# Kernel tuning notes

Hardware: AMD Instinct MI355X
Metric: run time of the kernel (lower is better)

The kernel has to match this reference:

```python
import jax, jax.numpy as jnp
import numpy as np

C = 256
CQK = C // 8  # query/key channels


def setup_inputs() -> dict:
    key = jax.random.key(0)
    ks = jax.random.split(key, 7)
    B, H, W = 4, 64, 64
    x = jax.random.normal(ks[0], (B, C, H, W), dtype=jnp.float32)
    # 1x1 conv weights stored as [out_ch, in_ch] (kernel spatial dims are 1)
    sc = 1.0 / np.sqrt(C)
    Wq = jax.random.uniform(ks[1], (CQK, C), jnp.float32, -sc, sc)
    bq = jax.random.uniform(ks[2], (CQK,), jnp.float32, -sc, sc)
    Wk = jax.random.uniform(ks[3], (CQK, C), jnp.float32, -sc, sc)
    bk = jax.random.uniform(ks[4], (CQK,), jnp.float32, -sc, sc)
    Wv = jax.random.uniform(ks[5], (C, C), jnp.float32, -sc, sc)
    bv = jax.random.uniform(ks[6], (C,), jnp.float32, -sc, sc)
    gamma = jnp.zeros((1,), dtype=jnp.float32)
    return {"x": x, "Wq": Wq, "bq": bq, "Wk": Wk, "bk": bk, "Wv": Wv, "bv": bv, "gamma": gamma}


def reference(x, Wq, bq, Wk, bk, Wv, bv, gamma):
    B, Ch, H, W = x.shape
    N = H * W
    xf = x.reshape(B, Ch, N)  # [B, C, N]
    # 1x1 convs == per-pixel linear projections
    q = jnp.einsum('oc,bcn->bno', Wq, xf) + bq  # [B, N, CQK]
    k = jnp.einsum('oc,bcn->bon', Wk, xf) + bk[None, :, None]  # [B, CQK, N]
    v = jnp.einsum('oc,bcn->bon', Wv, xf) + bv[None, :, None]  # [B, C, N]
    s = jnp.einsum('bnd,bdm->bnm', q, k)  # [B, N, N]
    attn = jax.nn.softmax(s, axis=-1)
    # out[b,c,i] = sum_j v[b,c,j] * attn[b,i,j]
    out = jnp.einsum('bcj,bij->bci', v, attn).reshape(B, Ch, H, W)
    return x + gamma[0] * out
```

## Files before the change

### kernel.cpp

```cpp
#include <hip/hip_runtime.h>
#include <math.h>

#define BATCH 4
#define CCH   256
#define DQK   32
#define NPIX  4096
#define LOG2E 1.44269504088896340736f

typedef __attribute__((ext_vector_type(8)))  short          short8_t;
typedef __attribute__((ext_vector_type(4)))  unsigned short ushort4_t;
typedef __attribute__((ext_vector_type(8)))  unsigned short ushort8_t;
typedef __attribute__((ext_vector_type(16))) float          f32x16;
typedef __attribute__((ext_vector_type(2)))  unsigned int   uint2_t;

#if __has_builtin(__builtin_amdgcn_exp2f)
#define EXP2F(x) __builtin_amdgcn_exp2f(x)
#else
#define EXP2F(x) exp2f(x)
#endif

#define MFMA32(a, b, c) __builtin_amdgcn_mfma_f32_32x32x16_bf16(a, b, c, 0, 0, 0)

static __device__ __forceinline__ unsigned short f2bf(float f) {
    union { float f; unsigned int u; } v; v.f = f;
    unsigned int r = v.u + 0x7FFFu + ((v.u >> 16) & 1u);
    return (unsigned short)(r >> 16);
}

static __device__ __forceinline__ short8_t cat8(ushort4_t a, ushort4_t b) {
    ushort8_t c = __builtin_shufflevector(a, b, 0, 1, 2, 3, 4, 5, 6, 7);
    short8_t r; __builtin_memcpy(&r, &c, 16); return r;
}

static __device__ __forceinline__ short8_t u4_to_s8(const unsigned int* u) {
    short8_t r; __builtin_memcpy(&r, u, 16); return r;
}

static __device__ __forceinline__ uint2_t plswap(unsigned int a, unsigned int b) {
#if __has_builtin(__builtin_amdgcn_permlane32_swap)
    return __builtin_amdgcn_permlane32_swap(a, b, false, false);
#else
    const unsigned int sa = (unsigned int)__shfl_xor((int)a, 32);
    const unsigned int sb = (unsigned int)__shfl_xor((int)b, 32);
    const int h = (threadIdx.x >> 5) & 1;
    uint2_t r;
    r.x = h ? sb : a;
    r.y = h ? b : sa;
    return r;
#endif
}

static __device__ __forceinline__ void make_bfrag(
    const f32x16& s, float& l0, float& l1, unsigned int bfr[2][4])
{
    float pv[16];
    #pragma unroll
    for (int r = 0; r < 16; ++r) pv[r] = EXP2F(s[r]);
    #pragma unroll
    for (int r = 0; r < 16; r += 2) { l0 += pv[r]; l1 += pv[r + 1]; }
    unsigned int P[8];
    #pragma unroll
    for (int v = 0; v < 8; ++v)
        P[v] = __builtin_amdgcn_perm(__float_as_uint(pv[2 * v + 1]),
                                     __float_as_uint(pv[2 * v]), 0x07060302u);
    #pragma unroll
    for (int kp = 0; kp < 2; ++kp) {
        const uint2_t r02 = plswap(P[4 * kp + 0], P[4 * kp + 2]);
        const uint2_t r13 = plswap(P[4 * kp + 1], P[4 * kp + 3]);
        bfr[kp][0] = r02.x; bfr[kp][1] = r13.x;
        bfr[kp][2] = r02.y; bfr[kp][3] = r13.y;
    }
}

__global__ __launch_bounds__(256) void wconv_kernel(
    const float* __restrict__ Wq, const float* __restrict__ Wk,
    const float* __restrict__ Wv, unsigned short* __restrict__ wbf)
{
    const int idx = blockIdx.x * 256 + threadIdx.x;
    const int o = idx >> 8, c = idx & 255;
    float v;
    if (o < 32)      v = Wq[o * 256 + c] * LOG2E;
    else if (o < 64) v = Wk[(o - 32) * 256 + c];
    else             v = Wv[(o - 64) * 256 + c];
    wbf[((c >> 3) * 320 + o) * 8 + (c & 7)] = f2bf(v);
}

__global__ __launch_bounds__(256) void xt_kernel(
    const float* __restrict__ x, unsigned short* __restrict__ xfrag)
{
    const int b  = blockIdx.x >> 6;
    const int cg = (blockIdx.x >> 4) & 3;
    const int ng = blockIdx.x & 15;
    const int t  = threadIdx.x;
    const int w = t >> 6, l = t & 63;

    #pragma unroll
    for (int sgl = 0; sgl < 2; ++sgl) {
        const int sg = w * 2 + sgl;
        float f[4][8];
        #pragma unroll
        for (int p = 0; p < 8; ++p) {
            const float* row = x + ((size_t)(b * CCH + cg * 64 + sg * 8 + p)) * NPIX
                                 + ng * 256;
            #pragma unroll
            for (int j = 0; j < 4; ++j)
                f[j][p] = row[j * 64 + l];
        }
        #pragma unroll
        for (int j = 0; j < 4; ++j) {
            unsigned int d[4];
            #pragma unroll
            for (int k = 0; k < 4; ++k)
                d[k] = __builtin_amdgcn_perm(__float_as_uint(f[j][2 * k + 1]),
                                             __float_as_uint(f[j][2 * k]), 0x07060302u);
            const int nt = ng * 8 + j * 2 + (l >> 5);
            unsigned short* dst = xfrag +
                ((((size_t)(b * 128 + nt) * 32) + cg * 8 + sg) * 32 + (l & 31)) * 8;
            *(short8_t*)dst = u4_to_s8(d);
        }
    }
}

__global__ __launch_bounds__(320) void proj_kernel(
    const unsigned short* __restrict__ xfrag, const unsigned short* __restrict__ wbf,
    const float* __restrict__ bq, const float* __restrict__ bk,
    const float* __restrict__ bv,
    unsigned short* __restrict__ qfrag, unsigned short* __restrict__ kfrag,
    unsigned short* __restrict__ vfrag)
{
    __shared__ unsigned short qkb[2 * 2 * 32 * 40];
    __shared__ unsigned short vbuf[4 * 64 * 72];

    const int b   = blockIdx.x >> 6;
    const int nt0 = (blockIdx.x & 63) << 1;
    const int t   = threadIdx.x;
    const int w = t >> 6, lane = t & 63, il = lane & 31, h = lane >> 5;

    float4 bA[4], bB[4];
    #pragma unroll
    for (int g = 0; g < 4; ++g) {
        if (w == 0) {
            bA[g] = *(const float4*)&bq[8 * g + 4 * h];
            bB[g] = *(const float4*)&bk[8 * g + 4 * h];
        } else {
            bA[g] = *(const float4*)&bv[(w - 1) * 64 + 8 * g + 4 * h];
            bB[g] = *(const float4*)&bv[(w - 1) * 64 + 32 + 8 * g + 4 * h];
        }
    }

    f32x16 acc[2][2];
    #pragma unroll
    for (int a = 0; a < 2; ++a)
        #pragma unroll
        for (int i = 0; i < 2; ++i)
            #pragma unroll
            for (int r = 0; r < 16; ++r) acc[a][i][r] = 0.f;

    const unsigned short* wp = wbf + ((size_t)(h * 320 + w * 64 + il)) * 8;
    const unsigned short* xp0 = xfrag + (((size_t)(b * 128 + nt0) * 32 + h) * 32 + il) * 8;
    const unsigned short* xp1 = xp0 + (size_t)32 * 32 * 8;

    #pragma unroll 4
    for (int ks = 0; ks < 16; ++ks) {
        const short8_t af0 = *(const short8_t*)(wp + ks * 5120);
        const short8_t af1 = *(const short8_t*)(wp + ks * 5120 + 256);
        const short8_t bf0 = *(const short8_t*)(xp0 + (size_t)ks * 2 * 256);
        const short8_t bf1 = *(const short8_t*)(xp1 + (size_t)ks * 2 * 256);
        acc[0][0] = MFMA32(af0, bf0, acc[0][0]);
        acc[0][1] = MFMA32(af0, bf1, acc[0][1]);
        acc[1][0] = MFMA32(af1, bf0, acc[1][0]);
        acc[1][1] = MFMA32(af1, bf1, acc[1][1]);
    }

    if (w == 0) {
        #pragma unroll
        for (int it = 0; it < 2; ++it)
            #pragma unroll
            for (int r = 0; r < 16; ++r) {
                const int d = (r & 3) + 8 * (r >> 2) + 4 * h;
                qkb[(it * 2 + 0) * 1280 + il * 40 + d] =
                    f2bf(acc[0][it][r] + bA[r >> 2][r & 3] * LOG2E);
                qkb[(it * 2 + 1) * 1280 + il * 40 + d] =
                    f2bf(acc[1][it][r] + bB[r >> 2][r & 3]);
            }
        #pragma unroll
        for (int it = 0; it < 2; ++it)
            #pragma unroll
            for (int rep = 0; rep < 2; ++rep) {
                const int u = rep * 64 + lane;
                const int slot = u >> 5, n = u & 31;
                ushort4_t qlo = *(const ushort4_t*)&qkb[(it * 2) * 1280 + n * 40 + slot * 8];
                ushort4_t qhi = *(const ushort4_t*)&qkb[(it * 2) * 1280 + n * 40 + slot * 8 + 4];
                ushort4_t klo = *(const ushort4_t*)&qkb[(it * 2 + 1) * 1280 + n * 40 + slot * 8];
                ushort4_t khi = *(const ushort4_t*)&qkb[(it * 2 + 1) * 1280 + n * 40 + slot * 8 + 4];
                const size_t o8 = (((size_t)(b * 128 + nt0 + it) * 4 + slot) * 32 + n) * 8;
                *(short8_t*)(qfrag + o8) = cat8(qlo, qhi);
                *(short8_t*)(kfrag + o8) = cat8(klo, khi);
            }
    } else {
        unsigned short* vb = vbuf + (w - 1) * 64 * 72;
        #pragma unroll
        for (int it = 0; it < 2; ++it)
            #pragma unroll
            for (int r = 0; r < 16; ++r) {
                const int orow = (r & 3) + 8 * (r >> 2) + 4 * h;
                vb[(orow)      * 72 + it * 32 + il] = f2bf(acc[0][it][r] + bA[r >> 2][r & 3]);
                vb[(orow + 32) * 72 + it * 32 + il] = f2bf(acc[1][it][r] + bB[r >> 2][r & 3]);
            }
        #pragma unroll
        for (int rep = 0; rep < 8; ++rep) {
            const int u = rep * 64 + lane;
            const int c = u & 63, m = u >> 6;
            const int it = m >> 2, slot = m & 3;
            ushort4_t lo = *(const ushort4_t*)&vb[c * 72 + it * 32 + slot * 8];
            ushort4_t hi = *(const ushort4_t*)&vb[c * 72 + it * 32 + slot * 8 + 4];
            const size_t o8 = (((size_t)(b * 128 + nt0 + it) * 4 + slot) * 256 +
                               (w - 1) * 64 + c) * 8;
            *(short8_t*)(vfrag + o8) = cat8(lo, hi);
        }
    }
}

struct KStage { short8_t k0, k1; };

__global__ __launch_bounds__(512, 2) void attn_kernel(
    const unsigned short* __restrict__ qfrag,
    const unsigned short* __restrict__ kfrag,
    const unsigned short* __restrict__ vfrag,
    const float* __restrict__ x,
    const float* __restrict__ gamma,
    float* __restrict__ out)
{
    __shared__ float comb[8][64][17];

    const int m8 = blockIdx.x & 7;
    const int b  = m8 >> 1;
    const int itile = ((blockIdx.x >> 3) << 1) | (m8 & 1);
    const int i0 = itile << 6;
    const int t  = threadIdx.x;
    const int w = t >> 6, lane = t & 63, il = lane & 31, h = lane >> 5;
    const int it = w & 1, ci = (w >> 1) & 1, jj = w >> 2;

    short8_t qf[2];
    #pragma unroll
    for (int ks = 0; ks < 2; ++ks)
        qf[ks] = *(const short8_t*)(qfrag +
            (((size_t)(b * 128 + itile * 2 + it) * 4 + ks * 2 + h) * 32 + il) * 8);

    const size_t kbase = (size_t)(b * 128 + jj * 64) * 1024 + h * 256 + il * 8;
    const size_t vbase = (size_t)(b * 128 + jj * 64) * 8192 + h * 2048 +
                         (ci * 128 + il) * 8;

    f32x16 zf;
    #pragma unroll
    for (int r = 0; r < 16; ++r) zf[r] = 0.f;
    f32x16 acc[4];
    #pragma unroll
    for (int c4 = 0; c4 < 4; ++c4) acc[c4] = zf;
    float ls[2] = {0.f, 0.f};

    KStage A, B;
    short8_t va[4][2], vb[4][2];

    auto loadK = [&](KStage& S, int jt) {
        const unsigned short* kp = kfrag + kbase + (size_t)jt * 1024;
        S.k0 = *(const short8_t*)kp;
        S.k1 = *(const short8_t*)(kp + 512);
    };
    auto loadV = [&](short8_t (&vv)[4][2], int jt) {
        const unsigned short* vp = vfrag + vbase + (size_t)jt * 8192;
        #pragma unroll
        for (int ct = 0; ct < 4; ++ct) {
            vv[ct][0] = *(const short8_t*)(vp + ct * 256);
            vv[ct][1] = *(const short8_t*)(vp + ct * 256 + 4096);
        }
    };

    loadK(A, 0);
    loadK(B, 1);
    loadV(va, 0);
    loadV(vb, 1);

    #pragma unroll 1
    for (int jt = 0; jt < 64; jt += 2) {
        f32x16 sA = MFMA32(A.k0, qf[0], zf);
        sA = MFMA32(A.k1, qf[1], sA);
        f32x16 sB = MFMA32(B.k0, qf[0], zf);
        sB = MFMA32(B.k1, qf[1], sB);
        if (jt + 2 < 64) loadK(A, jt + 2);
        if (jt + 3 < 64) loadK(B, jt + 3);

        unsigned int bfA[2][4];
        make_bfrag(sA, ls[0], ls[1], bfA);
        #pragma unroll
        for (int ct = 0; ct < 4; ++ct) {
            acc[ct] = MFMA32(va[ct][0], u4_to_s8(bfA[0]), acc[ct]);
            acc[ct] = MFMA32(va[ct][1], u4_to_s8(bfA[1]), acc[ct]);
        }
        unsigned int bfB[2][4];
        make_bfrag(sB, ls[0], ls[1], bfB);
        if (jt + 2 < 64) loadV(va, jt + 2);
        #pragma unroll
        for (int ct = 0; ct < 4; ++ct) {
            acc[ct] = MFMA32(vb[ct][0], u4_to_s8(bfB[0]), acc[ct]);
            acc[ct] = MFMA32(vb[ct][1], u4_to_s8(bfB[1]), acc[ct]);
        }
        if (jt + 3 < 64) loadV(vb, jt + 3);
    }

    float l = ls[0] + ls[1];
    l += __shfl_xor(l, 32);
    const float gam = gamma[0];
    const int pw = w ^ 4;
    float lt = 0.f;

    #pragma unroll
    for (int ct = 0; ct < 4; ++ct) {
        __syncthreads();
        #pragma unroll
        for (int r = 0; r < 16; ++r) comb[w][lane][r] = acc[ct][r];
        if (ct == 0) comb[w][lane][16] = l;
        __syncthreads();
        if (ct == 0) lt = l + comb[pw][lane][16];
        if ((ct >> 1) == jj) {
            const float sc = gam / lt;
            #pragma unroll
            for (int r = 0; r < 16; ++r) {
                const float o = acc[ct][r] + comb[pw][lane][r];
                const int c = ci * 128 + ct * 32 + (r & 3) + 8 * (r >> 2) + 4 * h;
                const size_t idx = ((size_t)(b * CCH + c)) * NPIX + i0 +
                                   it * 32 + il;
                out[idx] = x[idx] + o * sc;
            }
        }
    }
}

extern "C" void kernel_launch(void* const* d_in, const int* in_sizes, int n_in,
                              void* d_out, int out_size, void* d_ws, size_t ws_size,
                              hipStream_t stream) {
    const float* x     = (const float*)d_in[0];
    const float* Wq    = (const float*)d_in[1];
    const float* bq    = (const float*)d_in[2];
    const float* Wk    = (const float*)d_in[3];
    const float* bk    = (const float*)d_in[4];
    const float* Wv    = (const float*)d_in[5];
    const float* bv    = (const float*)d_in[6];
    const float* gamma = (const float*)d_in[7];
    float* out = (float*)d_out;

    unsigned short* ws    = (unsigned short*)d_ws;
    unsigned short* wbf   = ws;
    unsigned short* xfrag = ws + 81920;
    unsigned short* qfrag = xfrag + (size_t)4194304;
    unsigned short* kfrag = qfrag + (size_t)524288;
    unsigned short* vfrag = kfrag + (size_t)524288;

    wconv_kernel<<<dim3(320), dim3(256), 0, stream>>>(Wq, Wk, Wv, wbf);
    xt_kernel<<<dim3(256), dim3(256), 0, stream>>>(x, xfrag);
    proj_kernel<<<dim3(256), dim3(320), 0, stream>>>(
        xfrag, wbf, bq, bk, bv, qfrag, kfrag, vfrag);
    attn_kernel<<<dim3(256), dim3(512), 0, stream>>>(
        qfrag, kfrag, vfrag, x, gamma, out);
}
```

Before: 149.4 us.

## Halve attention query tile to 32 rows and double grid for occupancy

Measured after the change: 210.7 us. 1.41x slower.

```diff
diff --git a/kernel.cpp b/kernel.cpp
--- a/kernel.cpp
+++ b/kernel.cpp
@@ -223,7 +223,7 @@
 
 struct KStage { short8_t k0, k1; };
 
-__global__ __launch_bounds__(512, 2) void attn_kernel(
+__global__ __launch_bounds__(512, 4) void attn_kernel(
     const unsigned short* __restrict__ qfrag,
     const unsigned short* __restrict__ kfrag,
     const unsigned short* __restrict__ vfrag,
@@ -235,42 +235,41 @@
 
     const int m8 = blockIdx.x & 7;
     const int b  = m8 >> 1;
-    const int itile = ((blockIdx.x >> 3) << 1) | (m8 & 1);
-    const int i0 = itile << 6;
+    const int qt = ((blockIdx.x >> 3) << 1) | (m8 & 1);
+    const int i0 = qt << 5;
     const int t  = threadIdx.x;
     const int w = t >> 6, lane = t & 63, il = lane & 31, h = lane >> 5;
-    const int it = w & 1, ci = (w >> 1) & 1, jj = w >> 2;
+    const int ci = w & 3, jq = w >> 2;
 
     short8_t qf[2];
     #pragma unroll
     for (int ks = 0; ks < 2; ++ks)
         qf[ks] = *(const short8_t*)(qfrag +
-            (((size_t)(b * 128 + itile * 2 + it) * 4 + ks * 2 + h) * 32 + il) * 8);
-
-    const size_t kbase = (size_t)(b * 128 + jj * 64) * 1024 + h * 256 + il * 8;
-    const size_t vbase = (size_t)(b * 128 + jj * 64) * 8192 + h * 2048 +
-                         (ci * 128 + il) * 8;
+            (((size_t)(b * 128 + qt) * 4 + ks * 2 + h) * 32 + il) * 8);
+
+    const size_t kbase = (size_t)(b * 128 + jq * 64) * 1024 + h * 256 + il * 8;
+    const size_t vbase = (size_t)(b * 128 + jq * 64) * 8192 + h * 2048 +
+                         (ci * 64 + il) * 8;
 
     f32x16 zf;
     #pragma unroll
     for (int r = 0; r < 16; ++r) zf[r] = 0.f;
-    f32x16 acc[4];
-    #pragma unroll
-    for (int c4 = 0; c4 < 4; ++c4) acc[c4] = zf;
+    f32x16 acc[2];
+    acc[0] = zf; acc[1] = zf;
     float ls[2] = {0.f, 0.f};
 
     KStage A, B;
-    short8_t va[4][2], vb[4][2];
+    short8_t va[2][2], vb[2][2];
 
     auto loadK = [&](KStage& S, int jt) {
         const unsigned short* kp = kfrag + kbase + (size_t)jt * 1024;
         S.k0 = *(const short8_t*)kp;
         S.k1 = *(const short8_t*)(kp + 512);
     };
-    auto loadV = [&](short8_t (&vv)[4][2], int jt) {
+    auto loadV = [&](short8_t (&vv)[2][2], int jt) {
         const unsigned short* vp = vfrag + vbase + (size_t)jt * 8192;
         #pragma unroll
-        for (int ct = 0; ct < 4; ++ct) {
+        for (int ct = 0; ct < 2; ++ct) {
             vv[ct][0] = *(const short8_t*)(vp + ct * 256);
             vv[ct][1] = *(const short8_t*)(vp + ct * 256 + 4096);
         }
@@ -283,28 +282,24 @@
 
     #pragma unroll 1
     for (int jt = 0; jt < 64; jt += 2) {
-        f32x16 sA = MFMA32(A.k0, qf[0], zf);
-        sA = MFMA32(A.k1, qf[1], sA);
-        f32x16 sB = MFMA32(B.k0, qf[0], zf);
-        sB = MFMA32(B.k1, qf[1], sB);
+        f32x16 s = MFMA32(A.k0, qf[0], zf);
+        s = MFMA32(A.k1, qf[1], s);
         if (jt + 2 < 64) loadK(A, jt + 2);
+        unsigned int bf[2][4];
+        make_bfrag(s, ls[0], ls[1], bf);
+        acc[0] = MFMA32(va[0][0], u4_to_s8(bf[0]), acc[0]);
+        acc[0] = MFMA32(va[0][1], u4_to_s8(bf[1]), acc[0]);
+        acc[1] = MFMA32(va[1][0], u4_to_s8(bf[0]), acc[1]);
+        acc[1] = MFMA32(va[1][1], u4_to_s8(bf[1]), acc[1]);
+        if (jt + 2 < 64) loadV(va, jt + 2);
+        s = MFMA32(B.k0, qf[0], zf);
+        s = MFMA32(B.k1, qf[1], s);
         if (jt + 3 < 64) loadK(B, jt + 3);
-
-        unsigned int bfA[2][4];
-        make_bfrag(sA, ls[0], ls[1], bfA);
-        #pragma unroll
-        for (int ct = 0; ct < 4; ++ct) {
-            acc[ct] = MFMA32(va[ct][0], u4_to_s8(bfA[0]), acc[ct]);
-            acc[ct] = MFMA32(va[ct][1], u4_to_s8(bfA[1]), acc[ct]);
-        }
-        unsigned int bfB[2][4];
-        make_bfrag(sB, ls[0], ls[1], bfB);
-        if (jt + 2 < 64) loadV(va, jt + 2);
-        #pragma unroll
-        for (int ct = 0; ct < 4; ++ct) {
-            acc[ct] = MFMA32(vb[ct][0], u4_to_s8(bfB[0]), acc[ct]);
-            acc[ct] = MFMA32(vb[ct][1], u4_to_s8(bfB[1]), acc[ct]);
-        }
+        make_bfrag(s, ls[0], ls[1], bf);
+        acc[0] = MFMA32(vb[0][0], u4_to_s8(bf[0]), acc[0]);
+        acc[0] = MFMA32(vb[0][1], u4_to_s8(bf[1]), acc[0]);
+        acc[1] = MFMA32(vb[1][0], u4_to_s8(bf[0]), acc[1]);
+        acc[1] = MFMA32(vb[1][1], u4_to_s8(bf[1]), acc[1]);
         if (jt + 3 < 64) loadV(vb, jt + 3);
     }
 
@@ -315,21 +310,20 @@
     float lt = 0.f;
 
     #pragma unroll
-    for (int ct = 0; ct < 4; ++ct) {
+    for (int ct = 0; ct < 2; ++ct) {
         __syncthreads();
         #pragma unroll
         for (int r = 0; r < 16; ++r) comb[w][lane][r] = acc[ct][r];
         if (ct == 0) comb[w][lane][16] = l;
         __syncthreads();
         if (ct == 0) lt = l + comb[pw][lane][16];
-        if ((ct >> 1) == jj) {
+        if (jq == ct) {
             const float sc = gam / lt;
             #pragma unroll
             for (int r = 0; r < 16; ++r) {
                 const float o = acc[ct][r] + comb[pw][lane][r];
-                const int c = ci * 128 + ct * 32 + (r & 3) + 8 * (r >> 2) + 4 * h;
-                const size_t idx = ((size_t)(b * CCH + c)) * NPIX + i0 +
-                                   it * 32 + il;
+                const int c = ci * 64 + ct * 32 + (r & 3) + 8 * (r >> 2) + 4 * h;
+                const size_t idx = ((size_t)(b * CCH + c)) * NPIX + i0 + il;
                 out[idx] = x[idx] + o * sc;
             }
         }
@@ -360,6 +354,6 @@
     xt_kernel<<<dim3(256), dim3(256), 0, stream>>>(x, xfrag);
     proj_kernel<<<dim3(256), dim3(320), 0, stream>>>(
         xfrag, wbf, bq, bk, bv, qfrag, kfrag, vfrag);
-    attn_kernel<<<dim3(256), dim3(512), 0, stream>>>(
+    attn_kernel<<<dim3(512), dim3(512), 0, stream>>>(
         qfrag, kfrag, vfrag, x, gamma, out);
 }
```
